# Kernel optimization log

Hardware: AMD Instinct MI355X
Metric: run time of the kernel (lower is better)

## Reference

```python
import jax, jax.numpy as jnp
import numpy as np

EPS = 1e-8

def dice3(x, gamma, beta, alpha):
    # x: [B, L, C]; torch BatchNorm1d on transposed [B, C, L] normalizes per-channel over (B, L)
    mu = x.mean(axis=(0, 1))
    var = x.var(axis=(0, 1))  # biased, matches torch BN normalization
    xn = (x - mu) / jnp.sqrt(var + EPS) * gamma + beta
    p = jax.nn.sigmoid(xn)
    return alpha * (1.0 - p) * x + p * x

def dice2(x, gamma, beta, alpha):
    # x: [B, C]; BN per-channel over batch
    mu = x.mean(axis=0)
    var = x.var(axis=0)
    xn = (x - mu) / jnp.sqrt(var + EPS) * gamma + beta
    p = jax.nn.sigmoid(xn)
    return alpha * (1.0 - p) * x + p * x

def setup_inputs() -> dict:
    key = jax.random.key(0)
    ks = jax.random.split(key, 20)
    B, L, E = 16384, 10, 64
    N_USER = N_ITEM = 1000000
    H1, H2 = 64, 16        # LocalActivationUnit hidden_unit
    F1, F2 = 200, 80       # fc_layer hidden_units[:2]
    f32 = jnp.float32
    inp = {}
    inp['sparse_inputs'] = jax.random.randint(ks[0], (B, 2), 0, N_USER)
    inp['seqs'] = jax.random.randint(ks[1], (B, L), 0, N_ITEM)
    inp['user_table'] = jax.random.normal(ks[2], (N_USER, E), f32) * 0.02
    inp['item_table'] = jax.random.normal(ks[3], (N_ITEM, E), f32) * 0.02
    inp['his_table'] = jax.random.normal(ks[4], (N_ITEM, E), f32) * 0.02
    # LocalActivationUnit: Linear(4E->64), Dice(64,dim3), Linear(64->16), fc2 Linear(16->1)
    inp['W1'] = jax.random.normal(ks[5], (4 * E, H1), f32) * 0.05
    inp['b1'] = jnp.zeros((H1,), f32)
    inp['g1'] = jnp.ones((H1,), f32)
    inp['be1'] = jnp.zeros((H1,), f32)
    inp['a1'] = jnp.zeros((H1,), f32)
    inp['W2'] = jax.random.normal(ks[6], (H1, H2), f32) * 0.1
    inp['b2'] = jnp.zeros((H2,), f32)
    inp['Wf'] = jax.random.normal(ks[7], (H2, 1), f32) * 0.2
    inp['bf'] = jnp.zeros((1,), f32)
    # fc_layer: Linear(3E->200), Dice(200,dim2), Linear(200->80), Dice(80,dim2), Linear(80->1), sigmoid
    inp['Wa'] = jax.random.normal(ks[8], (3 * E, F1), f32) * 0.05
    inp['ba'] = jnp.zeros((F1,), f32)
    inp['ga'] = jnp.ones((F1,), f32)
    inp['bea'] = jnp.zeros((F1,), f32)
    inp['aa'] = jnp.zeros((F1,), f32)
    inp['Wb'] = jax.random.normal(ks[9], (F1, F2), f32) * 0.08
    inp['bb'] = jnp.zeros((F2,), f32)
    inp['gb'] = jnp.ones((F2,), f32)
    inp['beb'] = jnp.zeros((F2,), f32)
    inp['ab'] = jnp.zeros((F2,), f32)
    inp['Wc'] = jax.random.normal(ks[10], (F2, 1), f32) * 0.1
    inp['bc'] = jnp.zeros((1,), f32)
    return inp

def reference(sparse_inputs, seqs, user_table, item_table, his_table,
              W1, b1, g1, be1, a1, W2, b2, Wf, bf,
              Wa, ba, ga, bea, aa, Wb, bb, gb, beb, ab, Wc, bc):
    user_emb = user_table[sparse_inputs[:, 0]]          # [B, E]
    item_emb = item_table[sparse_inputs[:, 1]]          # [B, E]
    his = his_table[seqs]                               # [B, L, E]
    queries = jnp.broadcast_to(item_emb[:, None, :], his.shape)
    # concat+diff+product attention features: [B, L, 4E]
    ai = jnp.concatenate([queries, his, queries - his, queries * his], axis=-1)
    h = dice3(ai @ W1 + b1, g1, be1, a1)                # [B, L, 64]
    h = h @ W2 + b2                                     # [B, L, 16]
    score = (h @ Wf + bf)[..., 0]                       # [B, L]
    score = jnp.where(seqs == 0, 0.0, score)            # masked_fill
    pooled = jnp.einsum('bl,ble->be', score, his)       # weighted pooling
    cf = jnp.concatenate([item_emb, pooled, user_emb], axis=-1)  # [B, 3E]
    z = dice2(cf @ Wa + ba, ga, bea, aa)
    z = dice2(z @ Wb + bb, gb, beb, ab)
    out = jax.nn.sigmoid(z @ Wc + bc)                   # [B, 1]
    return out
```

## Files before the change

### kernel.cpp

```cpp
#include <hip/hip_runtime.h>
#include <hip/hip_bf16.h>

constexpr int B_   = 16384;
constexpr int L_   = 10;
constexpr int E_   = 64;
constexpr int BL_  = B_ * L_;
constexpr int K1K_ = 4 * E_;
constexpr int H1_  = 64;
constexpr int H2_  = 16;
constexpr int CF_  = 3 * E_;
constexpr int F1_  = 200;
constexpr int F2_  = 80;

constexpr long OFF_T1    = 0;
constexpr long OFF_SCORE = 10485760;
constexpr long OFF_CF    = 10649600;
constexpr long OFF_ACC   = 13795328;
constexpr long OFF_Z1    = 0;
constexpr long OFF_Z2    = 3276800;
constexpr int  ACC_N     = 688;

__device__ __forceinline__ float sigmoidf_(float x) {
    return 1.0f / (1.0f + __expf(-x));
}

__global__ __launch_bounds__(256) void k_init(float* __restrict__ acc) {
    int i = blockIdx.x * 256 + threadIdx.x;
    if (i < ACC_N) acc[i] = 0.0f;
}

__global__ __launch_bounds__(256) void k_gemm1(
    const int* __restrict__ sparse, const int* __restrict__ seqs,
    const float* __restrict__ item_t, const float* __restrict__ his_t,
    const float* __restrict__ W1, const float* __restrict__ b1,
    float* __restrict__ t1, float* __restrict__ sum1, float* __restrict__ ssq1)
{
    __shared__ float W1s[K1K_ * H1_];
    __shared__ float ais[16 * K1K_];
    int tid = threadIdx.x;
    for (int i = tid; i < K1K_ * H1_; i += 256) W1s[i] = W1[i];

    int jslot = tid & 15;
    int rslot = tid >> 4;
    int j0 = jslot * 4;
    float bb0 = b1[j0], bb1 = b1[j0 + 1], bb2 = b1[j0 + 2], bb3 = b1[j0 + 3];

    float ps0 = 0.f, ps1 = 0.f, ps2 = 0.f, ps3 = 0.f;
    float pq0 = 0.f, pq1 = 0.f, pq2 = 0.f, pq3 = 0.f;

    int ntile = BL_ / 16;
    for (int tile = blockIdx.x; tile < ntile; tile += gridDim.x) {
        int row0 = tile * 16;
        __syncthreads();
        for (int i = tid; i < 16 * 64; i += 256) {
            int r = i >> 6, k = i & 63;
            int row = row0 + r;
            int b = row / L_;
            int item = sparse[2 * b + 1];
            int hidx = seqs[row];
            float q = item_t[(long)item * 64 + k];
            float h = his_t[(long)hidx * 64 + k];
            float* a = &ais[r * 256];
            a[k] = q;
            a[64 + k] = h;
            a[128 + k] = q - h;
            a[192 + k] = q * h;
        }
        __syncthreads();

        const float* arow = &ais[rslot * 256];
        float a0 = bb0, a1 = bb1, a2 = bb2, a3 = bb3;
        #pragma unroll 4
        for (int k = 0; k < 256; k += 4) {
            float4 av = *(const float4*)(arow + k);
            float4 w0 = *(const float4*)(W1s + (k + 0) * 64 + j0);
            float4 w1 = *(const float4*)(W1s + (k + 1) * 64 + j0);
            float4 w2 = *(const float4*)(W1s + (k + 2) * 64 + j0);
            float4 w3 = *(const float4*)(W1s + (k + 3) * 64 + j0);
            a0 += av.x * w0.x + av.y * w1.x + av.z * w2.x + av.w * w3.x;
            a1 += av.x * w0.y + av.y * w1.y + av.z * w2.y + av.w * w3.y;
            a2 += av.x * w0.z + av.y * w1.z + av.z * w2.z + av.w * w3.z;
            a3 += av.x * w0.w + av.y * w1.w + av.z * w2.w + av.w * w3.w;
        }
        int row = row0 + rslot;
        float4 outv; outv.x = a0; outv.y = a1; outv.z = a2; outv.w = a3;
        *(float4*)(t1 + (long)row * 64 + j0) = outv;
        ps0 += a0; ps1 += a1; ps2 += a2; ps3 += a3;
        pq0 += a0 * a0; pq1 += a1 * a1; pq2 += a2 * a2; pq3 += a3 * a3;
    }

    __syncthreads();
    float* reds = ais;
    float* redq = ais + 1024;
    reds[rslot * 64 + j0 + 0] = ps0; reds[rslot * 64 + j0 + 1] = ps1;
    reds[rslot * 64 + j0 + 2] = ps2; reds[rslot * 64 + j0 + 3] = ps3;
    redq[rslot * 64 + j0 + 0] = pq0; redq[rslot * 64 + j0 + 1] = pq1;
    redq[rslot * 64 + j0 + 2] = pq2; redq[rslot * 64 + j0 + 3] = pq3;
    __syncthreads();
    if (tid < 64) {
        float s = 0.f, q = 0.f;
        #pragma unroll
        for (int r = 0; r < 16; r++) { s += reds[r * 64 + tid]; q += redq[r * 64 + tid]; }
        atomicAdd(&sum1[tid], s);
        atomicAdd(&ssq1[tid], q);
    }
}

__global__ __launch_bounds__(256) void k_score(
    const float* __restrict__ t1, const int* __restrict__ seqs,
    const float* __restrict__ sum1, const float* __restrict__ ssq1,
    const float* __restrict__ g1, const float* __restrict__ be1, const float* __restrict__ a1v,
    const float* __restrict__ W2, const float* __restrict__ b2,
    const float* __restrict__ Wf, const float* __restrict__ bfv,
    float* __restrict__ score)
{
    __shared__ float As[64], Bs[64], Al[64];
    __shared__ float W2s[64 * 16];
    __shared__ float Wfs[16], b2s[16];
    int tid = threadIdx.x;
    if (tid < 64) {
        float mu = sum1[tid] * (1.0f / BL_);
        float var = ssq1[tid] * (1.0f / BL_) - mu * mu;
        float rstd = rsqrtf(var + 1e-8f);
        float A = rstd * g1[tid];
        As[tid] = A;
        Bs[tid] = be1[tid] - mu * A;
        Al[tid] = a1v[tid];
    }
    for (int i = tid; i < 64 * 16; i += 256) W2s[i] = W2[i];
    if (tid < 16) { Wfs[tid] = Wf[tid]; b2s[tid] = b2[tid]; }
    __syncthreads();

    int row = blockIdx.x * 256 + tid;
    float h[16];
    #pragma unroll
    for (int n = 0; n < 16; n++) h[n] = b2s[n];
    const float* trow = t1 + (long)row * 64;
    #pragma unroll 4
    for (int jj = 0; jj < 64; jj += 4) {
        float4 x4 = *(const float4*)(trow + jj);
        float xs[4] = {x4.x, x4.y, x4.z, x4.w};
        #pragma unroll
        for (int u = 0; u < 4; u++) {
            int j = jj + u;
            float x = xs[u];
            float xn = x * As[j] + Bs[j];
            float p = sigmoidf_(xn);
            float al = Al[j];
            float d = x * (al + p * (1.0f - al));
            #pragma unroll
            for (int n = 0; n < 16; n++) h[n] += d * W2s[j * 16 + n];
        }
    }
    float sc = bfv[0];
    #pragma unroll
    for (int n = 0; n < 16; n++) sc += h[n] * Wfs[n];
    if (seqs[row] == 0) sc = 0.0f;
    score[row] = sc;
}

__global__ __launch_bounds__(256) void k_pool(
    const int* __restrict__ sparse, const int* __restrict__ seqs,
    const float* __restrict__ user_t, const float* __restrict__ item_t,
    const float* __restrict__ his_t,
    const float* __restrict__ score, float* __restrict__ cf)
{
    int tid = threadIdx.x;
    int b = blockIdx.x * 4 + (tid >> 6);
    int e = tid & 63;
    float acc = 0.0f;
    #pragma unroll
    for (int l = 0; l < L_; l++) {
        float s = score[b * L_ + l];
        int hidx = seqs[b * L_ + l];
        acc += s * his_t[(long)hidx * 64 + e];
    }
    int uidx = sparse[2 * b];
    int iidx = sparse[2 * b + 1];
    cf[(long)b * CF_ + e]        = item_t[(long)iidx * 64 + e];
    cf[(long)b * CF_ + 64 + e]   = acc;
    cf[(long)b * CF_ + 128 + e]  = user_t[(long)uidx * 64 + e];
}

__global__ __launch_bounds__(256) void k_z1(
    const float* __restrict__ cf, const float* __restrict__ Wa, const float* __restrict__ ba,
    float* __restrict__ z1, float* __restrict__ sumA, float* __restrict__ ssqA)
{
    __shared__ float cfs[16 * CF_];
    int tid = threadIdx.x;
    int n = tid;
    float bav = (n < F1_) ? ba[n] : 0.0f;
    float ps = 0.f, pq = 0.f;

    int ntile = B_ / 16;
    for (int tile = blockIdx.x; tile < ntile; tile += gridDim.x) {
        int row0 = tile * 16;
        __syncthreads();
        for (int i = tid; i < 16 * CF_; i += 256) cfs[i] = cf[(long)row0 * CF_ + i];
        __syncthreads();
        if (n < F1_) {
            float acc[16];
            #pragma unroll
            for (int r = 0; r < 16; r++) acc[r] = 0.0f;
            for (int k = 0; k < CF_; k += 4) {
                float w0 = Wa[(long)(k + 0) * F1_ + n];
                float w1 = Wa[(long)(k + 1) * F1_ + n];
                float w2 = Wa[(long)(k + 2) * F1_ + n];
                float w3 = Wa[(long)(k + 3) * F1_ + n];
                #pragma unroll
                for (int r = 0; r < 16; r++) {
                    float4 c4 = *(const float4*)&cfs[r * CF_ + k];
                    acc[r] += c4.x * w0 + c4.y * w1 + c4.z * w2 + c4.w * w3;
                }
            }
            #pragma unroll
            for (int r = 0; r < 16; r++) {
                float v = acc[r] + bav;
                z1[(long)(row0 + r) * F1_ + n] = v;
                ps += v; pq += v * v;
            }
        }
    }
    if (n < F1_) {
        atomicAdd(&sumA[n], ps);
        atomicAdd(&ssqA[n], pq);
    }
}

__global__ __launch_bounds__(320) void k_z2(
    const float* __restrict__ z1, const float* __restrict__ Wb, const float* __restrict__ bbv,
    const float* __restrict__ sumA, const float* __restrict__ ssqA,
    const float* __restrict__ ga, const float* __restrict__ bea, const float* __restrict__ aav,
    float* __restrict__ z2, float* __restrict__ sumB, float* __restrict__ ssqB)
{
    __shared__ float zs[16 * F1_];
    __shared__ float Aa[F1_], Ba[F1_], ala[F1_];
    int tid = threadIdx.x;
    if (tid < F1_) {
        float mu = sumA[tid] * (1.0f / B_);
        float var = ssqA[tid] * (1.0f / B_) - mu * mu;
        float rstd = rsqrtf(var + 1e-8f);
        float A = rstd * ga[tid];
        Aa[tid] = A;
        Ba[tid] = bea[tid] - mu * A;
        ala[tid] = aav[tid];
    }
    int n = tid % F2_;
    int rgrp = tid / F2_;
    float bbl = bbv[n];
    float ps = 0.f, pq = 0.f;

    int ntile = B_ / 16;
    for (int tile = blockIdx.x; tile < ntile; tile += gridDim.x) {
        int row0 = tile * 16;
        __syncthreads();
        for (int i = tid; i < 16 * F1_; i += 320) {
            int k = i % F1_;
            float x = z1[(long)row0 * F1_ + i];
            float xn = x * Aa[k] + Ba[k];
            float p = sigmoidf_(xn);
            float al = ala[k];
            zs[i] = x * (al + p * (1.0f - al));
        }
        __syncthreads();
        float acc[4] = {0.f, 0.f, 0.f, 0.f};
        for (int k = 0; k < F1_; k += 4) {
            float w0 = Wb[(long)(k + 0) * F2_ + n];
            float w1 = Wb[(long)(k + 1) * F2_ + n];
            float w2 = Wb[(long)(k + 2) * F2_ + n];
            float w3 = Wb[(long)(k + 3) * F2_ + n];
            #pragma unroll
            for (int rr = 0; rr < 4; rr++) {
                float4 c4 = *(const float4*)&zs[(rgrp * 4 + rr) * F1_ + k];
                acc[rr] += c4.x * w0 + c4.y * w1 + c4.z * w2 + c4.w * w3;
            }
        }
        #pragma unroll
        for (int rr = 0; rr < 4; rr++) {
            int row = row0 + rgrp * 4 + rr;
            float v = acc[rr] + bbl;
            z2[(long)row * F2_ + n] = v;
            ps += v; pq += v * v;
        }
    }
    atomicAdd(&sumB[n], ps);
    atomicAdd(&ssqB[n], pq);
}

__global__ __launch_bounds__(256) void k_out(
    const float* __restrict__ z2,
    const float* __restrict__ sumB, const float* __restrict__ ssqB,
    const float* __restrict__ gb, const float* __restrict__ beb, const float* __restrict__ abv,
    const float* __restrict__ Wc, const float* __restrict__ bc,
    float* __restrict__ out)
{
    __shared__ float Ab[F2_], Bb[F2_], alb[F2_], Wcs[F2_];
    int tid = threadIdx.x;
    if (tid < F2_) {
        float mu = sumB[tid] * (1.0f / B_);
        float var = ssqB[tid] * (1.0f / B_) - mu * mu;
        float rstd = rsqrtf(var + 1e-8f);
        float A = rstd * gb[tid];
        Ab[tid] = A;
        Bb[tid] = beb[tid] - mu * A;
        alb[tid] = abv[tid];
        Wcs[tid] = Wc[tid];
    }
    __syncthreads();
    int row = blockIdx.x * 256 + tid;
    const float* zrow = z2 + (long)row * F2_;
    float acc = bc[0];
    #pragma unroll 4
    for (int k = 0; k < F2_; k += 4) {
        float4 x4 = *(const float4*)(zrow + k);
        float xs[4] = {x4.x, x4.y, x4.z, x4.w};
        #pragma unroll
        for (int u = 0; u < 4; u++) {
            int kk = k + u;
            float x = xs[u];
            float xn = x * Ab[kk] + Bb[kk];
            float p = sigmoidf_(xn);
            float al = alb[kk];
            float d = x * (al + p * (1.0f - al));
            acc += d * Wcs[kk];
        }
    }
    out[row] = sigmoidf_(acc);
}

extern "C" void kernel_launch(void* const* d_in, const int* in_sizes, int n_in,
                              void* d_out, int out_size, void* d_ws, size_t ws_size,
                              hipStream_t stream) {
    const int*   sparse = (const int*)  d_in[0];
    const int*   seqs   = (const int*)  d_in[1];
    const float* user_t = (const float*)d_in[2];
    const float* item_t = (const float*)d_in[3];
    const float* his_t  = (const float*)d_in[4];
    const float* W1  = (const float*)d_in[5];
    const float* b1  = (const float*)d_in[6];
    const float* g1  = (const float*)d_in[7];
    const float* be1 = (const float*)d_in[8];
    const float* a1  = (const float*)d_in[9];
    const float* W2  = (const float*)d_in[10];
    const float* b2  = (const float*)d_in[11];
    const float* Wf  = (const float*)d_in[12];
    const float* bfv = (const float*)d_in[13];
    const float* Wa  = (const float*)d_in[14];
    const float* ba  = (const float*)d_in[15];
    const float* ga  = (const float*)d_in[16];
    const float* bea = (const float*)d_in[17];
    const float* aa  = (const float*)d_in[18];
    const float* Wb  = (const float*)d_in[19];
    const float* bb  = (const float*)d_in[20];
    const float* gb  = (const float*)d_in[21];
    const float* beb = (const float*)d_in[22];
    const float* ab  = (const float*)d_in[23];
    const float* Wc  = (const float*)d_in[24];
    const float* bc  = (const float*)d_in[25];

    float* ws    = (float*)d_ws;
    float* t1    = ws + OFF_T1;
    float* score = ws + OFF_SCORE;
    float* cf    = ws + OFF_CF;
    float* acc   = ws + OFF_ACC;
    float* sum1  = acc;
    float* ssq1  = acc + 64;
    float* sumA  = acc + 128;
    float* ssqA  = acc + 328;
    float* sumB  = acc + 528;
    float* ssqB  = acc + 608;
    float* z1    = ws + OFF_Z1;
    float* z2    = ws + OFF_Z2;
    float* out   = (float*)d_out;

    k_init<<<3, 256, 0, stream>>>(acc);
    k_gemm1<<<512, 256, 0, stream>>>(sparse, seqs, item_t, his_t, W1, b1, t1, sum1, ssq1);
    k_score<<<BL_ / 256, 256, 0, stream>>>(t1, seqs, sum1, ssq1, g1, be1, a1, W2, b2, Wf, bfv, score);
    k_pool<<<B_ / 4, 256, 0, stream>>>(sparse, seqs, user_t, item_t, his_t, score, cf);
    k_z1<<<512, 256, 0, stream>>>(cf, Wa, ba, z1, sumA, ssqA);
    k_z2<<<512, 320, 0, stream>>>(z1, Wb, bb, sumA, ssqA, ga, bea, aa, z2, sumB, ssqB);
    k_out<<<B_ / 256, 256, 0, stream>>>(z2, sumB, ssqB, gb, beb, ab, Wc, bc, out);
}
```

Baseline: 863.3 us.

## Use bf16 MFMA for attention GEMM with pre-transposed bf16 W1

Replaces the scalar FP32 GEMM for the attention layer (ai @ W1) with bf16 MFMA 16x16x32 instructions. k_init now also converts W1 to a transposed bf16 copy stored in the score workspace slot, which is overwritten later. Each wave keeps its W1 fragment in registers, and gathered embeddings are packed to bf16 in shared memory in 64-row tiles. This cuts ALU and LDS cost but lowers the precision of the features and weights to bf16.

```diff
diff --git a/kernel.cpp b/kernel.cpp
--- a/kernel.cpp
+++ b/kernel.cpp
@@ -5,7 +5,6 @@
 constexpr int L_   = 10;
 constexpr int E_   = 64;
 constexpr int BL_  = B_ * L_;
-constexpr int K1K_ = 4 * E_;
 constexpr int H1_  = 64;
 constexpr int H2_  = 16;
 constexpr int CF_  = 3 * E_;
@@ -20,87 +19,114 @@
 constexpr long OFF_Z2    = 3276800;
 constexpr int  ACC_N     = 688;
 
+typedef __bf16 bf16x8 __attribute__((ext_vector_type(8)));
+typedef float  f32x4  __attribute__((ext_vector_type(4)));
+
 __device__ __forceinline__ float sigmoidf_(float x) {
     return 1.0f / (1.0f + __expf(-x));
 }
 
-__global__ __launch_bounds__(256) void k_init(float* __restrict__ acc) {
+__device__ __forceinline__ unsigned short f2bf(float f) {
+    unsigned u = __float_as_uint(f);
+    unsigned r = (u + 0x7fffu + ((u >> 16) & 1u)) >> 16;
+    return (unsigned short)r;
+}
+__device__ __forceinline__ unsigned pk2(float a, float b) {
+    return (unsigned)f2bf(a) | ((unsigned)f2bf(b) << 16);
+}
+
+__global__ __launch_bounds__(256) void k_init(
+    float* __restrict__ acc, const float* __restrict__ W1,
+    unsigned short* __restrict__ W1t)
+{
     int i = blockIdx.x * 256 + threadIdx.x;
     if (i < ACC_N) acc[i] = 0.0f;
-}
-
+    int k = i >> 6, n = i & 63;
+    W1t[n * 256 + k] = f2bf(W1[i]);
+}
+
+constexpr int AROW = 132;
 __global__ __launch_bounds__(256) void k_gemm1(
     const int* __restrict__ sparse, const int* __restrict__ seqs,
     const float* __restrict__ item_t, const float* __restrict__ his_t,
-    const float* __restrict__ W1, const float* __restrict__ b1,
+    const unsigned short* __restrict__ W1t, const float* __restrict__ b1,
     float* __restrict__ t1, float* __restrict__ sum1, float* __restrict__ ssq1)
 {
-    __shared__ float W1s[K1K_ * H1_];
-    __shared__ float ais[16 * K1K_];
-    int tid = threadIdx.x;
-    for (int i = tid; i < K1K_ * H1_; i += 256) W1s[i] = W1[i];
-
-    int jslot = tid & 15;
-    int rslot = tid >> 4;
-    int j0 = jslot * 4;
-    float bb0 = b1[j0], bb1 = b1[j0 + 1], bb2 = b1[j0 + 2], bb3 = b1[j0 + 3];
-
-    float ps0 = 0.f, ps1 = 0.f, ps2 = 0.f, ps3 = 0.f;
-    float pq0 = 0.f, pq1 = 0.f, pq2 = 0.f, pq3 = 0.f;
-
-    int ntile = BL_ / 16;
-    for (int tile = blockIdx.x; tile < ntile; tile += gridDim.x) {
-        int row0 = tile * 16;
-        __syncthreads();
-        for (int i = tid; i < 16 * 64; i += 256) {
-            int r = i >> 6, k = i & 63;
+    __shared__ unsigned As[64 * AROW];
+    __shared__ float redS[4][64];
+    __shared__ float redQ[4][64];
+
+    int tid  = threadIdx.x;
+    int lane = tid & 63;
+    int wave = tid >> 6;
+    int m    = lane & 15;
+    int quad = (lane >> 4) & 3;
+    int colg = 16 * wave + m;
+
+    bf16x8 bfr[8];
+    {
+        const unsigned short* wp = W1t + (long)colg * 256 + quad * 8;
+        #pragma unroll
+        for (int kk = 0; kk < 8; kk++)
+            bfr[kk] = *(const bf16x8*)(wp + kk * 32);
+    }
+    float bias = b1[colg];
+    float ps = 0.0f, pq = 0.0f;
+
+    for (int tile = blockIdx.x; tile < BL_ / 64; tile += gridDim.x) {
+        int row0 = tile * 64;
+        __syncthreads();
+        #pragma unroll
+        for (int t = 0; t < 8; t++) {
+            int slot = t * 256 + tid;
+            int p = slot & 31;
+            int r = slot >> 5;
             int row = row0 + r;
-            int b = row / L_;
+            int b = (unsigned)row / 10u;
             int item = sparse[2 * b + 1];
             int hidx = seqs[row];
-            float q = item_t[(long)item * 64 + k];
-            float h = his_t[(long)hidx * 64 + k];
-            float* a = &ais[r * 256];
-            a[k] = q;
-            a[64 + k] = h;
-            a[128 + k] = q - h;
-            a[192 + k] = q * h;
-        }
-        __syncthreads();
-
-        const float* arow = &ais[rslot * 256];
-        float a0 = bb0, a1 = bb1, a2 = bb2, a3 = bb3;
-        #pragma unroll 4
-        for (int k = 0; k < 256; k += 4) {
-            float4 av = *(const float4*)(arow + k);
-            float4 w0 = *(const float4*)(W1s + (k + 0) * 64 + j0);
-            float4 w1 = *(const float4*)(W1s + (k + 1) * 64 + j0);
-            float4 w2 = *(const float4*)(W1s + (k + 2) * 64 + j0);
-            float4 w3 = *(const float4*)(W1s + (k + 3) * 64 + j0);
-            a0 += av.x * w0.x + av.y * w1.x + av.z * w2.x + av.w * w3.x;
-            a1 += av.x * w0.y + av.y * w1.y + av.z * w2.y + av.w * w3.y;
-            a2 += av.x * w0.z + av.y * w1.z + av.z * w2.z + av.w * w3.z;
-            a3 += av.x * w0.w + av.y * w1.w + av.z * w2.w + av.w * w3.w;
-        }
-        int row = row0 + rslot;
-        float4 outv; outv.x = a0; outv.y = a1; outv.z = a2; outv.w = a3;
-        *(float4*)(t1 + (long)row * 64 + j0) = outv;
-        ps0 += a0; ps1 += a1; ps2 += a2; ps3 += a3;
-        pq0 += a0 * a0; pq1 += a1 * a1; pq2 += a2 * a2; pq3 += a3 * a3;
+            float2 q2 = *(const float2*)(item_t + (long)item * 64 + 2 * p);
+            float2 h2 = *(const float2*)(his_t  + (long)hidx * 64 + 2 * p);
+            unsigned* a = &As[r * AROW];
+            a[p]      = pk2(q2.x, q2.y);
+            a[32 + p] = pk2(h2.x, h2.y);
+            a[64 + p] = pk2(q2.x - h2.x, q2.y - h2.y);
+            a[96 + p] = pk2(q2.x * h2.x, q2.y * h2.y);
+        }
+        __syncthreads();
+
+        f32x4 acc[4] = {{0,0,0,0},{0,0,0,0},{0,0,0,0},{0,0,0,0}};
+        #pragma unroll
+        for (int kk = 0; kk < 8; kk++) {
+            int aoff = kk * 16 + quad * 4;
+            bf16x8 a0 = *(const bf16x8*)&As[( 0 + m) * AROW + aoff];
+            bf16x8 a1 = *(const bf16x8*)&As[(16 + m) * AROW + aoff];
+            bf16x8 a2 = *(const bf16x8*)&As[(32 + m) * AROW + aoff];
+            bf16x8 a3 = *(const bf16x8*)&As[(48 + m) * AROW + aoff];
+            acc[0] = __builtin_amdgcn_mfma_f32_16x16x32_bf16(a0, bfr[kk], acc[0], 0, 0, 0);
+            acc[1] = __builtin_amdgcn_mfma_f32_16x16x32_bf16(a1, bfr[kk], acc[1], 0, 0, 0);
+            acc[2] = __builtin_amdgcn_mfma_f32_16x16x32_bf16(a2, bfr[kk], acc[2], 0, 0, 0);
+            acc[3] = __builtin_amdgcn_mfma_f32_16x16x32_bf16(a3, bfr[kk], acc[3], 0, 0, 0);
+        }
+        float* tb = t1 + (long)row0 * 64 + colg;
+        #pragma unroll
+        for (int rs = 0; rs < 4; rs++) {
+            #pragma unroll
+            for (int reg = 0; reg < 4; reg++) {
+                float v = acc[rs][reg] + bias;
+                tb[(16 * rs + quad * 4 + reg) * 64] = v;
+                ps += v; pq += v * v;
+            }
+        }
     }
 
     __syncthreads();
-    float* reds = ais;
-    float* redq = ais + 1024;
-    reds[rslot * 64 + j0 + 0] = ps0; reds[rslot * 64 + j0 + 1] = ps1;
-    reds[rslot * 64 + j0 + 2] = ps2; reds[rslot * 64 + j0 + 3] = ps3;
-    redq[rslot * 64 + j0 + 0] = pq0; redq[rslot * 64 + j0 + 1] = pq1;
-    redq[rslot * 64 + j0 + 2] = pq2; redq[rslot * 64 + j0 + 3] = pq3;
+    redS[quad][colg] = ps;
+    redQ[quad][colg] = pq;
     __syncthreads();
     if (tid < 64) {
-        float s = 0.f, q = 0.f;
-        #pragma unroll
-        for (int r = 0; r < 16; r++) { s += reds[r * 64 + tid]; q += redq[r * 64 + tid]; }
+        float s = redS[0][tid] + redS[1][tid] + redS[2][tid] + redS[3][tid];
+        float q = redQ[0][tid] + redQ[1][tid] + redQ[2][tid] + redQ[3][tid];
         atomicAdd(&sum1[tid], s);
         atomicAdd(&ssq1[tid], q);
     }
@@ -372,9 +398,10 @@
     float* z1    = ws + OFF_Z1;
     float* z2    = ws + OFF_Z2;
     float* out   = (float*)d_out;
-
-    k_init<<<3, 256, 0, stream>>>(acc);
-    k_gemm1<<<512, 256, 0, stream>>>(sparse, seqs, item_t, his_t, W1, b1, t1, sum1, ssq1);
+    unsigned short* W1t = (unsigned short*)(ws + OFF_SCORE);
+
+    k_init<<<64, 256, 0, stream>>>(acc, W1, W1t);
+    k_gemm1<<<1024, 256, 0, stream>>>(sparse, seqs, item_t, his_t, W1t, b1, t1, sum1, ssq1);
     k_score<<<BL_ / 256, 256, 0, stream>>>(t1, seqs, sum1, ssq1, g1, be1, a1, W2, b2, Wf, bfv, score);
     k_pool<<<B_ / 4, 256, 0, stream>>>(sparse, seqs, user_t, item_t, his_t, score, cf);
     k_z1<<<512, 256, 0, stream>>>(cf, Wa, ba, z1, sumA, ssqA);
```

Result: faster. 745.7 us (-13.6%).
